# Kernel optimization log

Measured on AMD Instinct MI355X. Metric: run time of the kernel, lower is better.

The kernel has to match this reference:

```python
import jax, jax.numpy as jnp
import numpy as np

B, C, H, W = 64, 8, 256, 256
OUT_C, K = 8, 3
IN_FEAT = 8  # Linear in_channels


def setup_inputs() -> dict:
    key = jax.random.key(0)
    k1, k2, k3, k4 = jax.random.split(key, 4)
    x = jax.random.normal(k1, (B, C, H, W), dtype=jnp.float32)
    dynamic_weights = jax.random.normal(k2, (B, C, IN_FEAT), dtype=jnp.float32)
    # kernel_generator: Linear(in_channels -> out_channels*k*k)
    lim = 1.0 / np.sqrt(IN_FEAT)
    Wg = jax.random.uniform(k3, (OUT_C * K * K, IN_FEAT), dtype=jnp.float32, minval=-lim, maxval=lim)
    bg = jax.random.uniform(k4, (OUT_C * K * K,), dtype=jnp.float32, minval=-lim, maxval=lim)
    return {"x": x, "dynamic_weights": dynamic_weights, "Wg": Wg, "bg": bg}


def reference(x, dynamic_weights, Wg, bg):
    b, c, h, w = x.shape
    # per-sample kernel generation: (B, C, in_feat) @ (in_feat, OUT_C*K*K)
    lin = jnp.einsum('bci,oi->bco', dynamic_weights, Wg) + bg  # (B, C, OUT_C*K*K)
    # torch .view(B, out_C, C, k, k) reinterprets the row-major buffer
    kernels = lin.reshape(b, OUT_C, c, K, K)
    # batch-as-groups grouped conv: input (1, B*C, H, W), kernel (B*OUT_C, C, K, K)
    x1 = x.reshape(1, b * c, h, w)
    kern = kernels.reshape(b * OUT_C, c, K, K)
    out = jax.lax.conv_general_dilated(
        x1, kern,
        window_strides=(1, 1),
        padding=((1, 1), (1, 1)),
        dimension_numbers=('NCHW', 'OIHW', 'NCHW'),
        feature_group_count=b,
    )
    return out.reshape(b, OUT_C, h, w)
```

## Files before the change

kernel.cpp:

```cpp
#include <hip/hip_runtime.h>


#define HC   65536
#define WW   256
#define RPB  8

__global__ __launch_bounds__(576) void gen_kernels(
    const float* __restrict__ dw,
    const float* __restrict__ Wg,
    const float* __restrict__ bg,
    float* __restrict__ kern)
{
    const int b = blockIdx.x;
    const int j = threadIdx.x;
    if (j >= 576) return;
    const int ic   = j / 72;
    const int rem  = j % 72;
    const int kh   = rem / 24;
    const int rem2 = rem % 24;
    const int kw   = rem2 / 8;
    const int oc   = rem2 % 8;
    const int o    = ic * 9 + kh * 3 + kw;

    const float* d = dw + b * 64 + oc * 8;
    const float* g = Wg + o * 8;
    float v = bg[o];
#pragma unroll
    for (int i = 0; i < 8; ++i) v = fmaf(d[i], g[i], v);
    kern[b * 576 + j] = v;
}

__global__ __launch_bounds__(256) void dyn_conv_ws(
    const float* __restrict__ x,
    const float* __restrict__ kern,
    float* __restrict__ out)
{
    const int b  = blockIdx.y;
    const int h0 = blockIdx.x * RPB;
    const int w  = threadIdx.x;

    const float* xb = x + (size_t)b * 8 * HC;
    const float* Kb = kern + b * 576;
    float*       ob = out + (size_t)b * 8 * HC;

    float acc[RPB][8];
#pragma unroll
    for (int r = 0; r < RPB; ++r)
#pragma unroll
        for (int oc = 0; oc < 8; ++oc) acc[r][oc] = 0.f;

#pragma unroll 1
    for (int ic = 0; ic < 8; ++ic) {
        float wk[72];
        const float* Kic = Kb + ic * 72;
#pragma unroll
        for (int t = 0; t < 72; ++t) wk[t] = Kic[t];

        const float* xch = xb + ic * HC;
#pragma unroll
        for (int ri = 0; ri < RPB + 2; ++ri) {
            const int row = h0 - 1 + ri;
            float xm = 0.f, xc = 0.f, xp = 0.f;
            if (row >= 0 && row < 256) {
                const float* xr = xch + row * WW;
                xc = xr[w];
                xm = (w > 0)   ? xr[w - 1] : 0.f;
                xp = (w < 255) ? xr[w + 1] : 0.f;
            }
#pragma unroll
            for (int kh = 0; kh < 3; ++kh) {
                const int ro = ri - kh;
                if (ro < 0 || ro >= RPB) continue;
                const float* wr = &wk[kh * 24];
#pragma unroll
                for (int oc = 0; oc < 8; ++oc) {
                    float a = acc[ro][oc];
                    a = fmaf(xm, wr[0 * 8 + oc], a);
                    a = fmaf(xc, wr[1 * 8 + oc], a);
                    a = fmaf(xp, wr[2 * 8 + oc], a);
                    acc[ro][oc] = a;
                }
            }
        }
    }

    const int hw0 = h0 * WW + w;
#pragma unroll
    for (int oc = 0; oc < 8; ++oc) {
        float* orow = ob + oc * HC + hw0;
#pragma unroll
        for (int r = 0; r < RPB; ++r) orow[r * WW] = acc[r][oc];
    }
}

__global__ __launch_bounds__(256) void dyn_conv_fused(
    const float* __restrict__ x,
    const float* __restrict__ dw,
    const float* __restrict__ Wg,
    const float* __restrict__ bg,
    float* __restrict__ out)
{
    __shared__ float kl[576];
    const int b  = blockIdx.y;
    const int h0 = blockIdx.x * RPB;
    const int w  = threadIdx.x;

    for (int j = threadIdx.x; j < 576; j += 256) {
        const int ic   = j / 72;
        const int rem  = j % 72;
        const int kh   = rem / 24;
        const int rem2 = rem % 24;
        const int kw   = rem2 / 8;
        const int oc   = rem2 % 8;
        const int o    = ic * 9 + kh * 3 + kw;
        const float* d = dw + b * 64 + oc * 8;
        const float* g = Wg + o * 8;
        float v = bg[o];
#pragma unroll
        for (int i = 0; i < 8; ++i) v = fmaf(d[i], g[i], v);
        kl[j] = v;
    }
    __syncthreads();

    const float* xb = x + (size_t)b * 8 * HC;
    float*       ob = out + (size_t)b * 8 * HC;

    float acc[RPB][8];
#pragma unroll
    for (int r = 0; r < RPB; ++r)
#pragma unroll
        for (int oc = 0; oc < 8; ++oc) acc[r][oc] = 0.f;

#pragma unroll 1
    for (int ic = 0; ic < 8; ++ic) {
        float wk[72];
        const float* Kic = &kl[ic * 72];
#pragma unroll
        for (int t = 0; t < 72; ++t) wk[t] = Kic[t];

        const float* xch = xb + ic * HC;
#pragma unroll
        for (int ri = 0; ri < RPB + 2; ++ri) {
            const int row = h0 - 1 + ri;
            float xm = 0.f, xc = 0.f, xp = 0.f;
            if (row >= 0 && row < 256) {
                const float* xr = xch + row * WW;
                xc = xr[w];
                xm = (w > 0)   ? xr[w - 1] : 0.f;
                xp = (w < 255) ? xr[w + 1] : 0.f;
            }
#pragma unroll
            for (int kh = 0; kh < 3; ++kh) {
                const int ro = ri - kh;
                if (ro < 0 || ro >= RPB) continue;
                const float* wr = &wk[kh * 24];
#pragma unroll
                for (int oc = 0; oc < 8; ++oc) {
                    float a = acc[ro][oc];
                    a = fmaf(xm, wr[0 * 8 + oc], a);
                    a = fmaf(xc, wr[1 * 8 + oc], a);
                    a = fmaf(xp, wr[2 * 8 + oc], a);
                    acc[ro][oc] = a;
                }
            }
        }
    }

    const int hw0 = h0 * WW + w;
#pragma unroll
    for (int oc = 0; oc < 8; ++oc) {
        float* orow = ob + oc * HC + hw0;
#pragma unroll
        for (int r = 0; r < RPB; ++r) orow[r * WW] = acc[r][oc];
    }
}

extern "C" void kernel_launch(void* const* d_in, const int* in_sizes, int n_in,
                              void* d_out, int out_size, void* d_ws, size_t ws_size,
                              hipStream_t stream) {
    const float* x  = (const float*)d_in[0];
    const float* dw = (const float*)d_in[1];
    const float* Wg = (const float*)d_in[2];
    const float* bg = (const float*)d_in[3];
    float* out = (float*)d_out;

    const dim3 grid(256 / RPB, 64);
    const dim3 block(256);

    if (ws_size >= (size_t)(64 * 576 * sizeof(float))) {
        float* kern = (float*)d_ws;
        gen_kernels<<<dim3(64), dim3(576), 0, stream>>>(dw, Wg, bg, kern);
        dyn_conv_ws<<<grid, block, 0, stream>>>(x, kern, out);
    } else {
        dyn_conv_fused<<<grid, block, 0, stream>>>(x, dw, Wg, bg, out);
    }
}
```

Measured before the change: 247.8 us.

## Retile conv so each thread computes four adjacent columns of one row

```diff
diff --git a/kernel.cpp b/kernel.cpp
--- a/kernel.cpp
+++ b/kernel.cpp
@@ -4,6 +4,8 @@
 #define HC   65536
 #define WW   256
 #define RPB  8
+
+typedef float floatx4 __attribute__((ext_vector_type(4)));
 
 __global__ __launch_bounds__(576) void gen_kernels(
     const float* __restrict__ dw,
@@ -30,24 +32,26 @@
     kern[b * 576 + j] = v;
 }
 
-__global__ __launch_bounds__(256) void dyn_conv_ws(
+__global__ __launch_bounds__(256, 8) void dyn_conv_v4(
     const float* __restrict__ x,
     const float* __restrict__ kern,
     float* __restrict__ out)
 {
-    const int b  = blockIdx.y;
-    const int h0 = blockIdx.x * RPB;
-    const int w  = threadIdx.x;
+    const int b    = blockIdx.y;
+    const int wv   = threadIdx.x >> 6;
+    const int lane = threadIdx.x & 63;
+    const int h    = blockIdx.x * 4 + wv;
+    const int w4   = lane << 2;
 
     const float* xb = x + (size_t)b * 8 * HC;
     const float* Kb = kern + b * 576;
     float*       ob = out + (size_t)b * 8 * HC;
 
-    float acc[RPB][8];
+    float acc[4][8];
 #pragma unroll
-    for (int r = 0; r < RPB; ++r)
+    for (int c = 0; c < 4; ++c)
 #pragma unroll
-        for (int oc = 0; oc < 8; ++oc) acc[r][oc] = 0.f;
+        for (int oc = 0; oc < 8; ++oc) acc[c][oc] = 0.f;
 
 #pragma unroll 1
     for (int ic = 0; ic < 8; ++ic) {
@@ -58,38 +62,37 @@
 
         const float* xch = xb + ic * HC;
 #pragma unroll
-        for (int ri = 0; ri < RPB + 2; ++ri) {
-            const int row = h0 - 1 + ri;
-            float xm = 0.f, xc = 0.f, xp = 0.f;
+        for (int kh = 0; kh < 3; ++kh) {
+            const int row = h - 1 + kh;
+            float x0 = 0.f, x1 = 0.f, x2 = 0.f, x3 = 0.f, xl = 0.f, xr = 0.f;
             if (row >= 0 && row < 256) {
-                const float* xr = xch + row * WW;
-                xc = xr[w];
-                xm = (w > 0)   ? xr[w - 1] : 0.f;
-                xp = (w < 255) ? xr[w + 1] : 0.f;
+                const float* xrow = xch + row * WW;
+                const floatx4 v = *reinterpret_cast<const floatx4*>(xrow + w4);
+                x0 = v.x; x1 = v.y; x2 = v.z; x3 = v.w;
+                xl = (w4 > 0)       ? xrow[w4 - 1] : 0.f;
+                xr = (w4 + 4 < WW)  ? xrow[w4 + 4] : 0.f;
             }
+            const float* wr = &wk[kh * 24];
 #pragma unroll
-            for (int kh = 0; kh < 3; ++kh) {
-                const int ro = ri - kh;
-                if (ro < 0 || ro >= RPB) continue;
-                const float* wr = &wk[kh * 24];
-#pragma unroll
-                for (int oc = 0; oc < 8; ++oc) {
-                    float a = acc[ro][oc];
-                    a = fmaf(xm, wr[0 * 8 + oc], a);
-                    a = fmaf(xc, wr[1 * 8 + oc], a);
-                    a = fmaf(xp, wr[2 * 8 + oc], a);
-                    acc[ro][oc] = a;
-                }
+            for (int oc = 0; oc < 8; ++oc) {
+                const float w0 = wr[oc];
+                const float w1 = wr[8 + oc];
+                const float w2 = wr[16 + oc];
+                acc[0][oc] = fmaf(xl, w0, fmaf(x0, w1, fmaf(x1, w2, acc[0][oc])));
+                acc[1][oc] = fmaf(x0, w0, fmaf(x1, w1, fmaf(x2, w2, acc[1][oc])));
+                acc[2][oc] = fmaf(x1, w0, fmaf(x2, w1, fmaf(x3, w2, acc[2][oc])));
+                acc[3][oc] = fmaf(x2, w0, fmaf(x3, w1, fmaf(xr, w2, acc[3][oc])));
             }
         }
     }
 
-    const int hw0 = h0 * WW + w;
+    const size_t o0 = (size_t)h * WW + w4;
 #pragma unroll
     for (int oc = 0; oc < 8; ++oc) {
-        float* orow = ob + oc * HC + hw0;
-#pragma unroll
-        for (int r = 0; r < RPB; ++r) orow[r * WW] = acc[r][oc];
+        floatx4 v;
+        v.x = acc[0][oc]; v.y = acc[1][oc]; v.z = acc[2][oc]; v.w = acc[3][oc];
+        __builtin_nontemporal_store(
+            v, reinterpret_cast<floatx4*>(ob + oc * HC + o0));
     }
 }
 
@@ -184,14 +187,13 @@
     const float* bg = (const float*)d_in[3];
     float* out = (float*)d_out;
 
-    const dim3 grid(256 / RPB, 64);
-    const dim3 block(256);
-
     if (ws_size >= (size_t)(64 * 576 * sizeof(float))) {
         float* kern = (float*)d_ws;
         gen_kernels<<<dim3(64), dim3(576), 0, stream>>>(dw, Wg, bg, kern);
-        dyn_conv_ws<<<grid, block, 0, stream>>>(x, kern, out);
+        const dim3 grid(256 / 4, 64);
+        dyn_conv_v4<<<grid, dim3(256), 0, stream>>>(x, kern, out);
     } else {
-        dyn_conv_fused<<<grid, block, 0, stream>>>(x, dw, Wg, bg, out);
+        const dim3 grid(256 / RPB, 64);
+        dyn_conv_fused<<<grid, dim3(256), 0, stream>>>(x, dw, Wg, bg, out);
     }
 }
```

After: 439.7 us. 1.77x slower.
